# Kernel tuning notes

Hardware: AMD Instinct MI355X
Metric: run time of the kernel (lower is better)

The kernel has to match this reference:

```python
import jax, jax.numpy as jnp
import numpy as np

XYZ_MIN = -1.0
XYZ_MAX = 1.0
MULTIRES = 4  # viewdirs positional-embedding frequencies


def trilerp(grid, pts):
    """Trilinear interpolation, align_corners=True, border clamp.
    grid: [C, X, Y, Z]; pts: [N, 3] in world coords. Returns [N, C]."""
    res = np.array(grid.shape[1:])  # (X, Y, Z)
    resf = jnp.asarray(res, dtype=pts.dtype)
    u = (pts - XYZ_MIN) / (XYZ_MAX - XYZ_MIN) * (resf - 1.0)  # [N,3] voxel coords
    u = jnp.clip(u, 0.0, resf - 1.0)
    i0 = jnp.clip(jnp.floor(u).astype(jnp.int32), 0, jnp.asarray(res - 2, dtype=jnp.int32))
    f = u - i0.astype(pts.dtype)  # [N,3] fractional offsets
    out = 0.0
    for dx in (0, 1):
        wx = f[:, 0] if dx else 1.0 - f[:, 0]
        for dy in (0, 1):
            wy = f[:, 1] if dy else 1.0 - f[:, 1]
            for dz in (0, 1):
                wz = f[:, 2] if dz else 1.0 - f[:, 2]
                g = grid[:, i0[:, 0] + dx, i0[:, 1] + dy, i0[:, 2] + dz]  # [C,N]
                out = out + (wx * wy * wz) * g
    return out.T  # [N,C]


def embed_viewdirs(v):
    """NeRF positional embedding: [v, sin(2^k v), cos(2^k v)] -> [N, 3+3*2*MULTIRES]."""
    freqs = 2.0 ** jnp.arange(MULTIRES, dtype=v.dtype)  # [F]
    ang = v[:, None, :] * freqs[None, :, None]  # [N,F,3]
    n = v.shape[0]
    return jnp.concatenate([v, jnp.sin(ang).reshape(n, -1), jnp.cos(ang).reshape(n, -1)], axis=-1)


def setup_inputs() -> dict:
    key = jax.random.key(0)
    ks = jax.random.split(key, 8)
    n = 2097152
    pts = jax.random.uniform(ks[0], (n, 3), jnp.float32, minval=XYZ_MIN, maxval=XYZ_MAX)
    vd = jax.random.normal(ks[1], (n, 3), jnp.float32)
    viewdirs = vd / jnp.linalg.norm(vd, axis=-1, keepdims=True)
    density_grid = jax.random.normal(ks[2], (1, 160, 160, 160), jnp.float32)
    color_grid = jax.random.normal(ks[3], (12, 160, 160, 160), jnp.float32)
    in_dim = 9 + 3 + 3 * 2 * MULTIRES  # k0_view (12-3) + viewdirs embed (27) = 36
    w0 = jax.random.normal(ks[4], (in_dim, 128), jnp.float32) * (1.0 / np.sqrt(in_dim))
    w1 = jax.random.normal(ks[5], (128, 128), jnp.float32) * (1.0 / np.sqrt(128))
    w2 = jax.random.normal(ks[6], (128, 3), jnp.float32) * (1.0 / np.sqrt(128))
    return {
        "pts": pts, "viewdirs": viewdirs,
        "density_grid": density_grid, "color_grid": color_grid,
        "w0": w0, "b0": jnp.zeros((128,), jnp.float32),
        "w1": w1, "b1": jnp.zeros((128,), jnp.float32),
        "w2": w2, "b2": jnp.zeros((3,), jnp.float32),
    }


def reference(pts, viewdirs, density_grid, color_grid, w0, b0, w1, b1, w2, b2):
    # density branch (use_densitynet=False -> raw interpolated density, channels=1)
    pts_density = trilerp(density_grid, pts)  # [N,1]
    # color branch with color_emission: k0 = [diffuse(3), view-dep(9)]
    k0 = trilerp(color_grid, pts)  # [N,12]
    k0_diffuse, k0_view = k0[:, :3], k0[:, 3:]
    feat = jnp.concatenate([k0_view, embed_viewdirs(viewdirs)], axis=-1)  # [N,36]
    h = jax.nn.relu(feat @ w0 + b0)
    h = jax.nn.relu(h @ w1 + b1)
    k0_logit = h @ w2 + b2  # [N,3]
    pts_color = jax.nn.sigmoid(k0_logit + k0_diffuse)
    return jnp.concatenate([pts_color, pts_density], axis=-1)  # [N,4]
```

## Files before the change

### kernel.cpp

```cpp
#include <hip/hip_runtime.h>
#include <hip/hip_bf16.h>
#include <math.h>

#define RES   160
#define RES2  (160*160)
#define RES3  (160*160*160)
#define TG_ELEMS ((size_t)RES3 * 16)
#define TG_BYTES (TG_ELEMS * 2)

#define BLOB_BYTES  47616
#define BLOB_SHORTS 22528
#define BLOB_FLOATS 640
#define A1_OFF      12288
#define B1P_OFF     45056
#define W2P_OFF     45568

typedef __attribute__((ext_vector_type(8)))  short s16x8;
typedef __attribute__((ext_vector_type(4)))  float f32x4;
typedef __attribute__((ext_vector_type(16))) float f32x16;
typedef __attribute__((ext_vector_type(4)))  int   i32x4;

__device__ __forceinline__ unsigned short f2bf(float x) {
    union { float f; unsigned u; } v; v.f = x;
    unsigned r = v.u + 0x7FFFu + ((v.u >> 16) & 1u);
    return (unsigned short)(r >> 16);
}
__device__ __forceinline__ unsigned pack2(float lo, float hi) {
    return (unsigned)f2bf(lo) | ((unsigned)f2bf(hi) << 16);
}
__device__ __forceinline__ float bf_lo(unsigned u) {
    union { unsigned u; float f; } v; v.u = u << 16; return v.f;
}
__device__ __forceinline__ float bf_hi(unsigned u) {
    union { unsigned u; float f; } v; v.u = u & 0xFFFF0000u; return v.f;
}
__device__ __forceinline__ unsigned cvtpk_relu(float a, float b) {
    float x = fmaxf(a, 0.0f), y = fmaxf(b, 0.0f);
    unsigned r;
    asm("v_cvt_pk_bf16_f32 %0, %1, %2" : "=v"(r) : "v"(x), "v"(y));
    return r;
}

__device__ __forceinline__ float blob_short_val(int i, const float* __restrict__ w0,
                                                const float* __restrict__ b0,
                                                const float* __restrict__ w1) {
    if (i < 6144) {
        int e = i & 7, s = i >> 3;
        int lo = s & 31, r = s >> 5;
        int hi = r & 1, t = r >> 1;
        int wm = t / 3, ks = t - wm * 3;
        int k = ks * 16 + hi * 8 + e, n = wm * 32 + lo;
        return k < 36 ? w0[k * 128 + n] : (k == 36 ? b0[n] : 0.0f);
    } else {
        int i2 = i - 6144;
        int e = i2 & 7, s = i2 >> 3;
        int lo = s & 31, r = s >> 5;
        int hi = r & 1, t = r >> 1;
        int wm = t >> 3, ks = t & 7;
        int k = ks * 16 + hi * 8 + e, n = wm * 32 + lo;
        return w1[k * 128 + n];
    }
}
__device__ __forceinline__ float blob_float_val(int j, const float* __restrict__ b1,
                                                const float* __restrict__ w2) {
    if (j < 128) {
        int c = j & 3, r = j >> 2, hi = r & 1, t = r >> 1;
        int g = t & 3, wm = t >> 2;
        return b1[wm * 32 + 8 * g + 4 * hi + c];
    } else {
        int j2 = j - 128;
        int cc = j2 & 3, m = j2 >> 2;
        int c = m & 3, r = m >> 2, hi = r & 1, t = r >> 1;
        int g = t & 3, wm = t >> 2;
        return cc < 3 ? w2[(wm * 32 + 8 * g + 4 * hi + c) * 3 + cc] : 0.0f;
    }
}

__global__ __launch_bounds__(256) void make_tg(
    const float* __restrict__ dgrid, const float* __restrict__ cgrid,
    short* __restrict__ tg)
{
    const int v = blockIdx.x * 256 + threadIdx.x;
    float vals[13];
    #pragma unroll
    for (int c = 0; c < 12; ++c) vals[c] = cgrid[(size_t)c * RES3 + v];
    vals[12] = dgrid[v];

    i32x4 r0 = { (int)pack2(vals[0], vals[1]),  (int)pack2(vals[2],  vals[3]),
                 (int)pack2(vals[4], vals[5]),  (int)pack2(vals[6],  vals[7]) };
    i32x4 r1 = { (int)pack2(vals[8], vals[9]),  (int)pack2(vals[10], vals[11]),
                 (int)pack2(vals[12], 0.0f),    0 };
    *(i32x4*)&tg[(size_t)v * 16 + 0] = r0;
    *(i32x4*)&tg[(size_t)v * 16 + 8] = r1;
}

__global__ __launch_bounds__(256) void prepack(
    const float* __restrict__ w0, const float* __restrict__ b0,
    const float* __restrict__ w1, const float* __restrict__ b1,
    const float* __restrict__ w2, char* __restrict__ blob)
{
    int t = blockIdx.x * 256 + threadIdx.x;
    if (t < BLOB_SHORTS) {
        ((short*)blob)[t] = (short)f2bf(blob_short_val(t, w0, b0, w1));
    } else if (t < BLOB_SHORTS + BLOB_FLOATS) {
        int j = t - BLOB_SHORTS;
        ((float*)(blob + B1P_OFF))[j] = blob_float_val(j, b1, w2);
    }
}

template<bool TG, bool PRE>
__global__ __launch_bounds__(256, 3) void dvgo_fused(
    const float* __restrict__ pts, const float* __restrict__ vdirs,
    const float* __restrict__ dgrid, const float* __restrict__ cgrid,
    const short* __restrict__ tg, const char* __restrict__ blob,
    const float* __restrict__ w0, const float* __restrict__ b0,
    const float* __restrict__ w1, const float* __restrict__ b1,
    const float* __restrict__ w2, const float* __restrict__ b2,
    float* __restrict__ out)
{
    __shared__ __align__(16) char smem[BLOB_BYTES];
    const int tid  = threadIdx.x;
    const int lane = tid & 63;
    const int wv   = tid >> 6;
    const int lo   = lane & 31;
    const int hi   = lane >> 5;

    if (PRE) {
        const i32x4* src = (const i32x4*)blob;
        i32x4* dst = (i32x4*)smem;
        for (int i = tid; i < BLOB_BYTES / 16; i += 256) dst[i] = src[i];
    } else {
        for (int i = tid; i < BLOB_SHORTS; i += 256)
            ((short*)smem)[i] = (short)f2bf(blob_short_val(i, w0, b0, w1));
        for (int i = tid; i < BLOB_FLOATS; i += 256)
            ((float*)(smem + B1P_OFF))[i] = blob_float_val(i, b1, w2);
    }

    const int p = blockIdx.x * 256 + tid;
    float P0 = pts[p*3+0], P1 = pts[p*3+1], P2 = pts[p*3+2];
    float V0 = vdirs[p*3+0], V1 = vdirs[p*3+1], V2 = vdirs[p*3+2];

    int   ii[3];
    float ff[3];
    float Pv[3] = {P0, P1, P2};
    #pragma unroll
    for (int d = 0; d < 3; ++d) {
        float u = (Pv[d] + 1.0f) * 79.5f;
        u = fminf(fmaxf(u, 0.0f), 159.0f);
        int i0 = (int)u;
        if (i0 > 158) i0 = 158;
        ii[d] = i0;
        ff[d] = u - (float)i0;
    }
    const float fx = ff[0], fy = ff[1], fz = ff[2];
    const float wxy0 = (1.0f-fx)*(1.0f-fy);
    const float wxy1 = (1.0f-fx)*fy;
    const float wxy2 = fx*(1.0f-fy);
    const float wxy3 = fx*fy;

    float dens;
    float col[12];

    if (TG) {
        const int base16 = ((ii[0]*RES + ii[1])*RES + ii[2]) * 16;
        const short* q00 = tg + base16;
        const short* q01 = q00 + RES*16;
        const short* q10 = q00 + RES2*16;
        const short* q11 = q10 + RES*16;

        float cv[13];
        #pragma unroll
        for (int c = 0; c < 13; ++c) cv[c] = 0.0f;

        const short* qs[4] = { q00, q01, q10, q11 };
        const float  ws[4] = { wxy0, wxy1, wxy2, wxy3 };
        #pragma unroll
        for (int cn = 0; cn < 4; ++cn) {
            const short* q = qs[cn];
            const float  w = ws[cn];
            i32x4 u0 = *(const i32x4*)(q);
            i32x4 u1 = *(const i32x4*)(q + 8);
            i32x4 u2 = *(const i32x4*)(q + 16);
            i32x4 u3 = *(const i32x4*)(q + 24);
            unsigned a[8] = { (unsigned)u0[0], (unsigned)u0[1], (unsigned)u0[2], (unsigned)u0[3],
                              (unsigned)u1[0], (unsigned)u1[1], (unsigned)u1[2], (unsigned)u1[3] };
            unsigned b[8] = { (unsigned)u2[0], (unsigned)u2[1], (unsigned)u2[2], (unsigned)u2[3],
                              (unsigned)u3[0], (unsigned)u3[1], (unsigned)u3[2], (unsigned)u3[3] };
            #pragma unroll
            for (int c = 0; c < 13; ++c) {
                float va = (c & 1) ? bf_hi(a[c >> 1]) : bf_lo(a[c >> 1]);
                float vb = (c & 1) ? bf_hi(b[c >> 1]) : bf_lo(b[c >> 1]);
                cv[c] += w * (va + fz * (vb - va));
            }
        }
        #pragma unroll
        for (int c = 0; c < 12; ++c) col[c] = cv[c];
        dens = cv[12];
    } else {
        const int base = (ii[0]*RES + ii[1])*RES + ii[2];
        const int o0 = base, o1 = base + RES, o2 = base + RES2, o3 = base + RES2 + RES;
        auto tl = [&](const float* __restrict__ g) -> float {
            float a0 = g[o0], a1 = g[o0+1];
            float c0 = g[o1], c1 = g[o1+1];
            float d0 = g[o2], d1 = g[o2+1];
            float e0 = g[o3], e1 = g[o3+1];
            float v0 = a0 + fz*(a1-a0);
            float v1 = c0 + fz*(c1-c0);
            float v2 = d0 + fz*(d1-d0);
            float v3 = e0 + fz*(e1-e0);
            return wxy0*v0 + wxy1*v1 + wxy2*v2 + wxy3*v3;
        };
        dens = tl(dgrid);
        #pragma unroll
        for (int c = 0; c < 12; ++c) col[c] = tl(cgrid + (size_t)c * RES3);
    }

    float ft[36];
    #pragma unroll
    for (int j = 0; j < 9; ++j) ft[j] = col[3+j];
    ft[9] = V0; ft[10] = V1; ft[11] = V2;
    float Vv[3] = {V0, V1, V2};
    #pragma unroll
    for (int k = 0; k < 4; ++k) {
        float s = (float)(1 << k);
        #pragma unroll
        for (int d = 0; d < 3; ++d) {
            float a = Vv[d] * s;
            ft[12 + 3*k + d] = __sinf(a);
            ft[24 + 3*k + d] = __cosf(a);
        }
    }
    unsigned fpk[24];
    #pragma unroll
    for (int j = 0; j < 18; ++j) fpk[j] = pack2(ft[2*j], ft[2*j+1]);
    fpk[18] = pack2(1.0f, 0.0f);
    #pragma unroll
    for (int j = 19; j < 24; ++j) fpk[j] = 0u;

    const float col0v = col[0], col1v = col[1], col2v = col[2];
    const float scol0 = __shfl_xor(col0v, 32, 64);
    const float scol1 = __shfl_xor(col1v, 32, 64);
    const float scol2 = __shfl_xor(col2v, 32, 64);
    const float sdens = __shfl_xor(dens,  32, 64);
    const float b2v0 = b2[0], b2v1 = b2[1], b2v2 = b2[2];

    __syncthreads();

    const char*  a0p  = smem + lane * 16;
    const char*  a1p  = smem + A1_OFF + lane * 16;
    const float* b1ph = (const float*)(smem + B1P_OFF) + hi * 4;
    const float* w2ph = (const float*)(smem + W2P_OFF) + hi * 16;

    #pragma unroll
    for (int pt = 0; pt < 2; ++pt) {
        f32x16 acc0[4];
        #pragma unroll
        for (int w = 0; w < 4; ++w)
            #pragma unroll
            for (int r = 0; r < 16; ++r) acc0[w][r] = 0.0f;

        #pragma unroll
        for (int ks = 0; ks < 3; ++ks) {
            unsigned bfr[4];
            #pragma unroll
            for (int d = 0; d < 4; ++d) {
                unsigned own_hi = fpk[ks*8 + 4 + d];
                unsigned own_lo = fpk[ks*8 + d];
                unsigned sw = (unsigned)__shfl_xor((int)(pt == 0 ? own_hi : own_lo), 32, 64);
                bfr[d] = (pt == 0) ? (hi ? sw : own_lo) : (hi ? own_hi : sw);
            }
            i32x4 bi = { (int)bfr[0], (int)bfr[1], (int)bfr[2], (int)bfr[3] };
            s16x8 B = __builtin_bit_cast(s16x8, bi);
            #pragma unroll
            for (int w = 0; w < 4; ++w) {
                s16x8 A = *(const s16x8*)(a0p + (w*3 + ks) * 1024);
                acc0[w] = __builtin_amdgcn_mfma_f32_32x32x16_bf16(A, B, acc0[w], 0, 0, 0);
            }
        }

        unsigned u1[4][8];
        #pragma unroll
        for (int w = 0; w < 4; ++w)
            #pragma unroll
            for (int g = 0; g < 4; ++g) {
                u1[w][2*g+0] = cvtpk_relu(acc0[w][4*g+0], acc0[w][4*g+1]);
                u1[w][2*g+1] = cvtpk_relu(acc0[w][4*g+2], acc0[w][4*g+3]);
            }

        f32x16 acc1[4];
        #pragma unroll
        for (int w = 0; w < 4; ++w)
            #pragma unroll
            for (int g = 0; g < 4; ++g) {
                f32x4 bv = *(const f32x4*)(b1ph + (w*4 + g) * 8);
                acc1[w][4*g+0] = bv[0]; acc1[w][4*g+1] = bv[1];
                acc1[w][4*g+2] = bv[2]; acc1[w][4*g+3] = bv[3];
            }
        #pragma unroll
        for (int ks = 0; ks < 8; ++ks) {
            const int wsrc = ks >> 1, q = 4 * (ks & 1);
            unsigned su[4];
            #pragma unroll
            for (int i = 0; i < 4; ++i)
                su[i] = (unsigned)__shfl_xor((int)u1[wsrc][q + i], 32, 64);
            unsigned bfr[4];
            bfr[0] = hi ? su[2]            : u1[wsrc][q+0];
            bfr[1] = hi ? su[3]            : u1[wsrc][q+1];
            bfr[2] = hi ? u1[wsrc][q+2]    : su[0];
            bfr[3] = hi ? u1[wsrc][q+3]    : su[1];
            i32x4 bi = { (int)bfr[0], (int)bfr[1], (int)bfr[2], (int)bfr[3] };
            s16x8 B = __builtin_bit_cast(s16x8, bi);
            #pragma unroll
            for (int w = 0; w < 4; ++w) {
                s16x8 A = *(const s16x8*)(a1p + (w*8 + ks) * 1024);
                acc1[w] = __builtin_amdgcn_mfma_f32_32x32x16_bf16(A, B, acc1[w], 0, 0, 0);
            }
        }

        float p0 = 0.0f, p1 = 0.0f, p2 = 0.0f;
        #pragma unroll
        for (int w = 0; w < 4; ++w)
            #pragma unroll
            for (int g = 0; g < 4; ++g) {
                const float* wrow = w2ph + (w*4 + g) * 32;
                #pragma unroll
                for (int c = 0; c < 4; ++c) {
                    float v = fmaxf(acc1[w][4*g+c], 0.0f);
                    f32x4 wvv = *(const f32x4*)(wrow + c * 4);
                    p0 += v * wvv[0]; p1 += v * wvv[1]; p2 += v * wvv[2];
                }
            }
        p0 += __shfl_xor(p0, 32, 64);
        p1 += __shfl_xor(p1, 32, 64);
        p2 += __shfl_xor(p2, 32, 64);

        const float d0 = pt ? scol0 : col0v;
        const float d1 = pt ? scol1 : col1v;
        const float d2 = pt ? scol2 : col2v;
        const float dn = pt ? sdens : dens;
        if (hi == 0) {
            float x0 = p0 + b2v0 + d0;
            float x1 = p1 + b2v1 + d1;
            float x2 = p2 + b2v2 + d2;
            f32x4 o = { 1.0f / (1.0f + __expf(-x0)),
                        1.0f / (1.0f + __expf(-x1)),
                        1.0f / (1.0f + __expf(-x2)),
                        dn };
            const int gp = blockIdx.x * 256 + wv * 64 + pt * 32 + lo;
            *(f32x4*)(out + (size_t)gp * 4) = o;
        }
    }
}

extern "C" void kernel_launch(void* const* d_in, const int* in_sizes, int n_in,
                              void* d_out, int out_size, void* d_ws, size_t ws_size,
                              hipStream_t stream) {
    const float* pts = (const float*)d_in[0];
    const float* vd  = (const float*)d_in[1];
    const float* dg  = (const float*)d_in[2];
    const float* cg  = (const float*)d_in[3];
    const float* w0  = (const float*)d_in[4];
    const float* b0  = (const float*)d_in[5];
    const float* w1  = (const float*)d_in[6];
    const float* b1  = (const float*)d_in[7];
    const float* w2  = (const float*)d_in[8];
    const float* b2  = (const float*)d_in[9];
    float* out = (float*)d_out;

    const int n = in_sizes[0] / 3;
    const int blocks = n / 256;

    if (ws_size >= TG_BYTES + BLOB_BYTES) {
        short* tg = (short*)d_ws;
        char* blob = (char*)d_ws + TG_BYTES;
        make_tg<<<RES3/256, 256, 0, stream>>>(dg, cg, tg);
        prepack<<<(BLOB_SHORTS + BLOB_FLOATS + 255)/256, 256, 0, stream>>>(w0, b0, w1, b1, w2, blob);
        dvgo_fused<true, true><<<blocks, 256, 0, stream>>>(
            pts, vd, dg, cg, tg, blob, w0, b0, w1, b1, w2, b2, out);
    } else if (ws_size >= TG_BYTES) {
        short* tg = (short*)d_ws;
        make_tg<<<RES3/256, 256, 0, stream>>>(dg, cg, tg);
        dvgo_fused<true, false><<<blocks, 256, 0, stream>>>(
            pts, vd, dg, cg, tg, nullptr, w0, b0, w1, b1, w2, b2, out);
    } else {
        dvgo_fused<false, false><<<blocks, 256, 0, stream>>>(
            pts, vd, dg, cg, nullptr, nullptr, w0, b0, w1, b1, w2, b2, out);
    }
}
```

Baseline: 287.8 us.

## Use packed FP32 math, permlane32 swaps, and sincos double-angle recurrences

Replaces the cross-half-wave __shfl_xor exchanges for the MFMA B operands and the final reduction with v_permlane32_swap, which avoids ds_bpermute traffic through LDS. The trilinear blend and the last-layer dot product now use v_pk_fma/v_pk_mul on pairs of channels. The packed W2 layout drops its zero padding to match. Software bf16 rounding is swapped for the hardware v_cvt_pk_bf16_f32 instruction. The 24 sin/cos calls per point become 3 sincos calls plus double-angle recurrences. This trims VALU and LDS-shuffle work per point, with some added rounding error from the recurrences.

```diff
diff --git a/kernel.cpp b/kernel.cpp
--- a/kernel.cpp
+++ b/kernel.cpp
@@ -8,14 +8,15 @@
 #define TG_ELEMS ((size_t)RES3 * 16)
 #define TG_BYTES (TG_ELEMS * 2)
 
-#define BLOB_BYTES  47616
+#define BLOB_BYTES  47104
 #define BLOB_SHORTS 22528
-#define BLOB_FLOATS 640
+#define BLOB_FLOATS 512
 #define A1_OFF      12288
 #define B1P_OFF     45056
 #define W2P_OFF     45568
 
 typedef __attribute__((ext_vector_type(8)))  short s16x8;
+typedef __attribute__((ext_vector_type(2)))  float f32x2;
 typedef __attribute__((ext_vector_type(4)))  float f32x4;
 typedef __attribute__((ext_vector_type(16))) float f32x16;
 typedef __attribute__((ext_vector_type(4)))  int   i32x4;
@@ -25,8 +26,10 @@
     unsigned r = v.u + 0x7FFFu + ((v.u >> 16) & 1u);
     return (unsigned short)(r >> 16);
 }
-__device__ __forceinline__ unsigned pack2(float lo, float hi) {
-    return (unsigned)f2bf(lo) | ((unsigned)f2bf(hi) << 16);
+__device__ __forceinline__ unsigned cvtpk(float lo, float hi) {
+    unsigned r;
+    asm("v_cvt_pk_bf16_f32 %0, %1, %2" : "=v"(r) : "v"(lo), "v"(hi));
+    return r;
 }
 __device__ __forceinline__ float bf_lo(unsigned u) {
     union { unsigned u; float f; } v; v.u = u << 16; return v.f;
@@ -35,9 +38,24 @@
     union { unsigned u; float f; } v; v.u = u & 0xFFFF0000u; return v.f;
 }
 __device__ __forceinline__ unsigned cvtpk_relu(float a, float b) {
-    float x = fmaxf(a, 0.0f), y = fmaxf(b, 0.0f);
-    unsigned r;
-    asm("v_cvt_pk_bf16_f32 %0, %1, %2" : "=v"(r) : "v"(x), "v"(y));
+    return cvtpk(fmaxf(a, 0.0f), fmaxf(b, 0.0f));
+}
+__device__ __forceinline__ void plswap(unsigned &a, unsigned &b) {
+    asm("v_permlane32_swap_b32 %0, %1" : "+v"(a), "+v"(b));
+}
+__device__ __forceinline__ float sum_halves(float x) {
+    unsigned a = __float_as_uint(x), b = a;
+    plswap(a, b);
+    return __uint_as_float(a) + __uint_as_float(b);
+}
+__device__ __forceinline__ f32x2 pkfma(f32x2 a, f32x2 b, f32x2 c) {
+    f32x2 r;
+    asm("v_pk_fma_f32 %0, %1, %2, %3" : "=v"(r) : "v"(a), "v"(b), "v"(c));
+    return r;
+}
+__device__ __forceinline__ f32x2 pkmul(f32x2 a, f32x2 b) {
+    f32x2 r;
+    asm("v_pk_mul_f32 %0, %1, %2" : "=v"(r) : "v"(a), "v"(b));
     return r;
 }
 
@@ -69,10 +87,13 @@
         return b1[wm * 32 + 8 * g + 4 * hi + c];
     } else {
         int j2 = j - 128;
-        int cc = j2 & 3, m = j2 >> 2;
-        int c = m & 3, r = m >> 2, hi = r & 1, t = r >> 1;
-        int g = t & 3, wm = t >> 2;
-        return cc < 3 ? w2[(wm * 32 + 8 * g + 4 * hi + c) * 3 + cc] : 0.0f;
+        int c  = j2 & 3;
+        int t  = j2 >> 2;
+        int cc = t % 3;
+        int u  = t / 3;
+        int hi = u & 1, v = u >> 1;
+        int g  = v & 3, wm = v >> 2;
+        return w2[(wm * 32 + 8 * g + 4 * hi + c) * 3 + cc];
     }
 }
 
@@ -86,10 +107,10 @@
     for (int c = 0; c < 12; ++c) vals[c] = cgrid[(size_t)c * RES3 + v];
     vals[12] = dgrid[v];
 
-    i32x4 r0 = { (int)pack2(vals[0], vals[1]),  (int)pack2(vals[2],  vals[3]),
-                 (int)pack2(vals[4], vals[5]),  (int)pack2(vals[6],  vals[7]) };
-    i32x4 r1 = { (int)pack2(vals[8], vals[9]),  (int)pack2(vals[10], vals[11]),
-                 (int)pack2(vals[12], 0.0f),    0 };
+    i32x4 r0 = { (int)cvtpk(vals[0], vals[1]),  (int)cvtpk(vals[2],  vals[3]),
+                 (int)cvtpk(vals[4], vals[5]),  (int)cvtpk(vals[6],  vals[7]) };
+    i32x4 r1 = { (int)cvtpk(vals[8], vals[9]),  (int)cvtpk(vals[10], vals[11]),
+                 (int)cvtpk(vals[12], 0.0f),    0 };
     *(i32x4*)&tg[(size_t)v * 16 + 0] = r0;
     *(i32x4*)&tg[(size_t)v * 16 + 8] = r1;
 }
@@ -168,34 +189,38 @@
         const short* q10 = q00 + RES2*16;
         const short* q11 = q10 + RES*16;
 
-        float cv[13];
-        #pragma unroll
-        for (int c = 0; c < 13; ++c) cv[c] = 0.0f;
+        f32x2 cv[7];
+        #pragma unroll
+        for (int pr = 0; pr < 7; ++pr) cv[pr] = f32x2{0.0f, 0.0f};
+
+        const f32x2 fzv   = { fz, fz };
+        const f32x2 omfzv = { 1.0f - fz, 1.0f - fz };
 
         const short* qs[4] = { q00, q01, q10, q11 };
-        const float  ws[4] = { wxy0, wxy1, wxy2, wxy3 };
+        const float  wsx[4] = { wxy0, wxy1, wxy2, wxy3 };
         #pragma unroll
         for (int cn = 0; cn < 4; ++cn) {
             const short* q = qs[cn];
-            const float  w = ws[cn];
             i32x4 u0 = *(const i32x4*)(q);
-            i32x4 u1 = *(const i32x4*)(q + 8);
+            i32x4 u1v = *(const i32x4*)(q + 8);
             i32x4 u2 = *(const i32x4*)(q + 16);
             i32x4 u3 = *(const i32x4*)(q + 24);
-            unsigned a[8] = { (unsigned)u0[0], (unsigned)u0[1], (unsigned)u0[2], (unsigned)u0[3],
-                              (unsigned)u1[0], (unsigned)u1[1], (unsigned)u1[2], (unsigned)u1[3] };
-            unsigned b[8] = { (unsigned)u2[0], (unsigned)u2[1], (unsigned)u2[2], (unsigned)u2[3],
-                              (unsigned)u3[0], (unsigned)u3[1], (unsigned)u3[2], (unsigned)u3[3] };
-            #pragma unroll
-            for (int c = 0; c < 13; ++c) {
-                float va = (c & 1) ? bf_hi(a[c >> 1]) : bf_lo(a[c >> 1]);
-                float vb = (c & 1) ? bf_hi(b[c >> 1]) : bf_lo(b[c >> 1]);
-                cv[c] += w * (va + fz * (vb - va));
+            unsigned av[8] = { (unsigned)u0[0], (unsigned)u0[1], (unsigned)u0[2], (unsigned)u0[3],
+                               (unsigned)u1v[0], (unsigned)u1v[1], (unsigned)u1v[2], (unsigned)u1v[3] };
+            unsigned bv[8] = { (unsigned)u2[0], (unsigned)u2[1], (unsigned)u2[2], (unsigned)u2[3],
+                               (unsigned)u3[0], (unsigned)u3[1], (unsigned)u3[2], (unsigned)u3[3] };
+            const f32x2 wv2 = { wsx[cn], wsx[cn] };
+            #pragma unroll
+            for (int pr = 0; pr < 7; ++pr) {
+                f32x2 va = { bf_lo(av[pr]), bf_hi(av[pr]) };
+                f32x2 vb = { bf_lo(bv[pr]), bf_hi(bv[pr]) };
+                f32x2 lz = pkfma(fzv, vb, pkmul(omfzv, va));
+                cv[pr] = pkfma(wv2, lz, cv[pr]);
             }
         }
         #pragma unroll
-        for (int c = 0; c < 12; ++c) col[c] = cv[c];
-        dens = cv[12];
+        for (int c = 0; c < 12; ++c) col[c] = (c & 1) ? cv[c >> 1].y : cv[c >> 1].x;
+        dens = cv[6].x;
     } else {
         const int base = (ii[0]*RES + ii[1])*RES + ii[2];
         const int o0 = base, o1 = base + RES, o2 = base + RES2, o3 = base + RES2 + RES;
@@ -221,21 +246,27 @@
     ft[9] = V0; ft[10] = V1; ft[11] = V2;
     float Vv[3] = {V0, V1, V2};
     #pragma unroll
-    for (int k = 0; k < 4; ++k) {
-        float s = (float)(1 << k);
-        #pragma unroll
-        for (int d = 0; d < 3; ++d) {
-            float a = Vv[d] * s;
-            ft[12 + 3*k + d] = __sinf(a);
-            ft[24 + 3*k + d] = __cosf(a);
-        }
+    for (int d = 0; d < 3; ++d) {
+        float s1, c1;
+        __sincosf(Vv[d], &s1, &c1);
+        float s2 = 2.0f*s1*c1,  c2 = __builtin_fmaf(-2.0f*s1, s1, 1.0f);
+        float s4 = 2.0f*s2*c2,  c4 = __builtin_fmaf(-2.0f*s2, s2, 1.0f);
+        float s8 = 2.0f*s4*c4,  c8 = __builtin_fmaf(-2.0f*s4, s4, 1.0f);
+        ft[12 + d] = s1; ft[15 + d] = s2; ft[18 + d] = s4; ft[21 + d] = s8;
+        ft[24 + d] = c1; ft[27 + d] = c2; ft[30 + d] = c4; ft[33 + d] = c8;
     }
     unsigned fpk[24];
     #pragma unroll
-    for (int j = 0; j < 18; ++j) fpk[j] = pack2(ft[2*j], ft[2*j+1]);
-    fpk[18] = pack2(1.0f, 0.0f);
+    for (int j = 0; j < 18; ++j) fpk[j] = cvtpk(ft[2*j], ft[2*j+1]);
+    fpk[18] = cvtpk(1.0f, 0.0f);
     #pragma unroll
     for (int j = 19; j < 24; ++j) fpk[j] = 0u;
+
+    #pragma unroll
+    for (int ks = 0; ks < 3; ++ks)
+        #pragma unroll
+        for (int d = 0; d < 4; ++d)
+            plswap(fpk[ks*8 + d], fpk[ks*8 + 4 + d]);
 
     const float col0v = col[0], col1v = col[1], col2v = col[2];
     const float scol0 = __shfl_xor(col0v, 32, 64);
@@ -249,7 +280,7 @@
     const char*  a0p  = smem + lane * 16;
     const char*  a1p  = smem + A1_OFF + lane * 16;
     const float* b1ph = (const float*)(smem + B1P_OFF) + hi * 4;
-    const float* w2ph = (const float*)(smem + W2P_OFF) + hi * 16;
+    const float* w2ph = (const float*)(smem + W2P_OFF) + hi * 12;
 
     #pragma unroll
     for (int pt = 0; pt < 2; ++pt) {
@@ -261,15 +292,8 @@
 
         #pragma unroll
         for (int ks = 0; ks < 3; ++ks) {
-            unsigned bfr[4];
-            #pragma unroll
-            for (int d = 0; d < 4; ++d) {
-                unsigned own_hi = fpk[ks*8 + 4 + d];
-                unsigned own_lo = fpk[ks*8 + d];
-                unsigned sw = (unsigned)__shfl_xor((int)(pt == 0 ? own_hi : own_lo), 32, 64);
-                bfr[d] = (pt == 0) ? (hi ? sw : own_lo) : (hi ? own_hi : sw);
-            }
-            i32x4 bi = { (int)bfr[0], (int)bfr[1], (int)bfr[2], (int)bfr[3] };
+            i32x4 bi = { (int)fpk[ks*8 + 4*pt + 0], (int)fpk[ks*8 + 4*pt + 1],
+                         (int)fpk[ks*8 + 4*pt + 2], (int)fpk[ks*8 + 4*pt + 3] };
             s16x8 B = __builtin_bit_cast(s16x8, bi);
             #pragma unroll
             for (int w = 0; w < 4; ++w) {
@@ -298,41 +322,40 @@
             }
         #pragma unroll
         for (int ks = 0; ks < 8; ++ks) {
-            const int wsrc = ks >> 1, q = 4 * (ks & 1);
-            unsigned su[4];
-            #pragma unroll
-            for (int i = 0; i < 4; ++i)
-                su[i] = (unsigned)__shfl_xor((int)u1[wsrc][q + i], 32, 64);
-            unsigned bfr[4];
-            bfr[0] = hi ? su[2]            : u1[wsrc][q+0];
-            bfr[1] = hi ? su[3]            : u1[wsrc][q+1];
-            bfr[2] = hi ? u1[wsrc][q+2]    : su[0];
-            bfr[3] = hi ? u1[wsrc][q+3]    : su[1];
-            i32x4 bi = { (int)bfr[0], (int)bfr[1], (int)bfr[2], (int)bfr[3] };
+            const int w = ks >> 1, q = 4 * (ks & 1);
+            plswap(u1[w][q+0], u1[w][q+2]);
+            plswap(u1[w][q+1], u1[w][q+3]);
+            i32x4 bi = { (int)u1[w][q+0], (int)u1[w][q+1],
+                         (int)u1[w][q+2], (int)u1[w][q+3] };
             s16x8 B = __builtin_bit_cast(s16x8, bi);
             #pragma unroll
-            for (int w = 0; w < 4; ++w) {
-                s16x8 A = *(const s16x8*)(a1p + (w*8 + ks) * 1024);
-                acc1[w] = __builtin_amdgcn_mfma_f32_32x32x16_bf16(A, B, acc1[w], 0, 0, 0);
+            for (int wm = 0; wm < 4; ++wm) {
+                s16x8 A = *(const s16x8*)(a1p + (wm*8 + ks) * 1024);
+                acc1[wm] = __builtin_amdgcn_mfma_f32_32x32x16_bf16(A, B, acc1[wm], 0, 0, 0);
             }
         }
 
-        float p0 = 0.0f, p1 = 0.0f, p2 = 0.0f;
+        f32x2 pa0 = {0.0f, 0.0f}, pa1 = {0.0f, 0.0f}, pa2 = {0.0f, 0.0f};
         #pragma unroll
         for (int w = 0; w < 4; ++w)
             #pragma unroll
             for (int g = 0; g < 4; ++g) {
-                const float* wrow = w2ph + (w*4 + g) * 32;
-                #pragma unroll
-                for (int c = 0; c < 4; ++c) {
-                    float v = fmaxf(acc1[w][4*g+c], 0.0f);
-                    f32x4 wvv = *(const f32x4*)(wrow + c * 4);
-                    p0 += v * wvv[0]; p1 += v * wvv[1]; p2 += v * wvv[2];
-                }
-            }
-        p0 += __shfl_xor(p0, 32, 64);
-        p1 += __shfl_xor(p1, 32, 64);
-        p2 += __shfl_xor(p2, 32, 64);
+                const float* wrow = w2ph + (w*4 + g) * 24;
+                f32x4 q0 = *(const f32x4*)(wrow + 0);
+                f32x4 q1 = *(const f32x4*)(wrow + 4);
+                f32x4 q2 = *(const f32x4*)(wrow + 8);
+                f32x2 v01 = { fmaxf(acc1[w][4*g+0], 0.0f), fmaxf(acc1[w][4*g+1], 0.0f) };
+                f32x2 v23 = { fmaxf(acc1[w][4*g+2], 0.0f), fmaxf(acc1[w][4*g+3], 0.0f) };
+                pa0 = pkfma(v01, f32x2{q0[0], q0[1]}, pa0);
+                pa0 = pkfma(v23, f32x2{q0[2], q0[3]}, pa0);
+                pa1 = pkfma(v01, f32x2{q1[0], q1[1]}, pa1);
+                pa1 = pkfma(v23, f32x2{q1[2], q1[3]}, pa1);
+                pa2 = pkfma(v01, f32x2{q2[0], q2[1]}, pa2);
+                pa2 = pkfma(v23, f32x2{q2[2], q2[3]}, pa2);
+            }
+        float p0 = sum_halves(pa0.x + pa0.y);
+        float p1 = sum_halves(pa1.x + pa1.y);
+        float p2 = sum_halves(pa2.x + pa2.y);
 
         const float d0 = pt ? scol0 : col0v;
         const float d1 = pt ? scol1 : col1v;
```

Measured after the change: 271.7 us. 5.6% less time.
